# Kernel optimization log

Hardware: AMD Instinct MI355X
Metric: run time of the kernel (lower is better)

Reference implementation:

```python
import jax, jax.numpy as jnp
import numpy as np

L = 2048           # lattice side
R = 2.777          # public-goods multiplier r
GAMMA = 0.8
ETA = 0.8
K_FERMI = 0.5      # fermi temperature used in fermiUpdate


def _plus_sum(x):
    """3x3 plus-kernel conv with circular (wrap) padding == self + 4 rolled neighbors."""
    return (x
            + jnp.roll(x, 1, 0) + jnp.roll(x, -1, 0)
            + jnp.roll(x, 1, 1) + jnp.roll(x, -1, 1))


def setup_inputs() -> dict:
    key = jax.random.key(0)
    k1, k2, k3, k4, k5 = jax.random.split(key, 5)
    return {
        "type_t_minus": jax.random.randint(k1, (L, L), 0, 2, dtype=jnp.int32),
        "type_t": jax.random.randint(k2, (L, L), 0, 2, dtype=jnp.int32),
        "Q_tensor": jax.random.normal(k3, (L * L, 2, 2), dtype=jnp.float32),
        "learning_direction": jax.random.randint(k4, (L, L), 0, 4, dtype=jnp.int32),
        "learning_probabilities": jax.random.uniform(k5, (L, L), dtype=jnp.float32),
    }


def reference(type_t_minus, type_t, Q_tensor, learning_direction, learning_probabilities):
    N = L * L
    # ---- calculation_value: per-cell payoff from the 5 overlapping PGG games ----
    c = (type_t == 1).astype(jnp.float32)   # cooperator mask
    d = (type_t == 0).astype(jnp.float32)   # defector mask
    coop_num = _plus_sum(c)                  # cooperators in own 5-cell group
    base = coop_num * (R / 5.0)
    profit = _plus_sum(base - 1.0) * c + _plus_sum(base) * d   # [L, L]

    # ---- updateQMatrix: Q[C, A, B] <- (1-eta)*Q[C,A,B] + eta*(profit + gamma*max_b Q[C,B,b]) ----
    A = type_t_minus.reshape(-1)             # previous action, [N]
    B = type_t.reshape(-1)                   # current action,  [N]
    Qb = jnp.take_along_axis(Q_tensor, B[:, None, None], axis=1)[:, 0, :]  # Q[C, B, :] -> [N, 2]
    max_values = Qb.max(axis=1)              # [N]
    flatQ = Q_tensor.reshape(N, 4)
    idx = A * 2 + B                          # flattened (A, B) index
    old = jnp.take_along_axis(flatQ, idx[:, None], axis=1)[:, 0]
    upd = (1.0 - ETA) * old + ETA * (profit.reshape(-1) + GAMMA * max_values)
    Q_new = flatQ.at[jnp.arange(N), idx].set(upd).reshape(N, 2, 2)

    # ---- fermiUpdate: gather just-updated Q[C,A,B] (== upd), compare with 4 neighbors ----
    pm = upd.reshape(L, L)                   # fermi profit matrix

    def W(shift, axis):
        return 1.0 / (1.0 + jnp.exp((pm - jnp.roll(pm, shift, axis)) / K_FERMI))

    Ws = jnp.stack([W(1, 1), W(-1, 1), W(1, 0), W(-1, 0)])        # left,right,up,down [4,L,L]
    nb = jnp.stack([jnp.roll(type_t, 1, 1), jnp.roll(type_t, -1, 1),
                    jnp.roll(type_t, 1, 0), jnp.roll(type_t, -1, 0)])
    W_sel = jnp.take_along_axis(Ws, learning_direction[None], axis=0)[0]
    nb_sel = jnp.take_along_axis(nb, learning_direction[None], axis=0)[0]
    type_t1 = jnp.where(learning_probabilities <= W_sel, nb_sel, type_t)  # [L, L] int32

    return (Q_new, type_t1, profit)
```

## Files before the change

kernel.cpp:

```cpp
#include <hip/hip_runtime.h>


#define LSIDE 2048
#define LMASK 2047
#define LSHIFT 11
#define NCELL (LSIDE * LSIDE)

#define TROWS 7
#define TCOLS 264
#define BROWS 5
#define BCOLS 260

__global__ __launch_bounds__(256) void spgg_fused(
    const int* __restrict__ tmin,
    const int* __restrict__ tt,
    const float* __restrict__ Q,
    const int* __restrict__ ldir,
    const float* __restrict__ lp,
    float* __restrict__ Qn,
    float* __restrict__ prof,
    float* __restrict__ t1out)
{
    __shared__ int   tile[TROWS][TCOLS];
    __shared__ float btile[BROWS][BCOLS];

    const int t   = threadIdx.x;
    const int blk = blockIdx.x;
    const int i   = blk >> 3;
    const int j0  = (blk & 7) << 8;
    const int j   = j0 + t;
    const int idx = (i << LSHIFT) + j;

    const int    dir = ldir[idx];
    const float  pv  = lp[idx];
    const float4 qr  = ((const float4*)Q)[idx];
    const int    A   = tmin[idx];

    for (int k = t; k < TROWS * (TCOLS / 4); k += 256) {
        int r = k / (TCOLS / 4);
        int m = k - r * (TCOLS / 4);
        int row_g = (i + r - 3) & LMASK;
        int col_g = (j0 - 4 + (m << 2)) & LMASK;
        int4 v = *(const int4*)&tt[(row_g << LSHIFT) + col_g];
        *(int4*)&tile[r][m << 2] = v;
    }

    const int di = (dir == 3) - (dir == 2);
    const int dj = (dir == 1) - (dir == 0);
    const int ni = (i + di) & LMASK;
    const int nj = (j + dj) & LMASK;
    const int nidx = (ni << LSHIFT) + nj;
    const float4 qn4 = ((const float4*)Q)[nidx];
    const int    An  = tmin[nidx];

    __syncthreads();

    const float KB        = 0.5554f;
    const float ETA       = 0.8f;
    const float ONE_M_ETA = 0.2f;
    const float GAMMA     = 0.8f;

    auto bval = [&](int tr, int tc) -> float {
        int cn = tile[tr][tc] + tile[tr-1][tc] + tile[tr+1][tc]
               + tile[tr][tc-1] + tile[tr][tc+1];
        return __fmul_rn((float)cn, KB);
    };
    #pragma unroll
    for (int r = 0; r < BROWS; ++r)
        btile[r][t] = bval(r + 1, t + 2);
    if (t < BCOLS - 256) {
        #pragma unroll
        for (int r = 0; r < BROWS; ++r)
            btile[r][256 + t] = bval(r + 1, 258 + t);
    }
    __syncthreads();

    auto profit_from_b = [&](int r, int c, int coop) -> float {
        float b_c = btile[r][c];
        float b_u = btile[r-1][c];
        float b_d = btile[r+1][c];
        float b_l = btile[r][c-1];
        float b_r = btile[r][c+1];
        float s0 = __fadd_rn(__fadd_rn(__fadd_rn(__fadd_rn(b_c, b_u), b_d), b_l), b_r);
        float s1 = __fadd_rn(__fadd_rn(__fadd_rn(__fadd_rn(
                       __fsub_rn(b_c, 1.0f), __fsub_rn(b_u, 1.0f)),
                       __fsub_rn(b_d, 1.0f)), __fsub_rn(b_l, 1.0f)),
                       __fsub_rn(b_r, 1.0f));
        return coop ? s1 : s0;
    };

    auto upd_of = [&](float profit, float4 q4, int Ai, int Bi) -> float {
        float q0 = (Bi == 0) ? q4.x : q4.z;
        float q1 = (Bi == 0) ? q4.y : q4.w;
        float mx = fmaxf(q0, q1);
        int k = Ai * 2 + Bi;
        float old = (k == 0) ? q4.x : ((k == 1) ? q4.y : ((k == 2) ? q4.z : q4.w));
        float t0 = __fmul_rn(GAMMA, mx);
        float t1 = __fadd_rn(profit, t0);
        float t2 = __fmul_rn(ETA, t1);
        float t3 = __fmul_rn(ONE_M_ETA, old);
        return __fadd_rn(t3, t2);
    };

    const int B     = tile[3][t + 4];
    float p_own = profit_from_b(2, t + 2, B);
    float upd   = upd_of(p_own, qr, A, B);

    int k = A * 2 + B;
    float4 qo;
    qo.x = (k == 0) ? upd : qr.x;
    qo.y = (k == 1) ? upd : qr.y;
    qo.z = (k == 2) ? upd : qr.z;
    qo.w = (k == 3) ? upd : qr.w;
    ((float4*)Qn)[idx] = qo;
    prof[idx] = p_own;

    const int Bn = tile[3 + di][t + 4 + dj];
    float p_nb   = profit_from_b(2 + di, t + 2 + dj, Bn);
    float upd_nb = upd_of(p_nb, qn4, An, Bn);

    float e1 = __fsub_rn(upd, upd_nb);
    float e2 = __fmul_rn(e1, 2.0f);
    float ex = (float)exp((double)e2);
    float W  = __fdiv_rn(1.0f, __fadd_rn(1.0f, ex));
    int sel = (pv <= W) ? Bn : B;
    t1out[idx] = (float)sel;
}

extern "C" void kernel_launch(void* const* d_in, const int* in_sizes, int n_in,
                              void* d_out, int out_size, void* d_ws, size_t ws_size,
                              hipStream_t stream) {
    const int*   type_t_minus = (const int*)d_in[0];
    const int*   type_t       = (const int*)d_in[1];
    const float* Q_tensor     = (const float*)d_in[2];
    const int*   ldir         = (const int*)d_in[3];
    const float* lprob        = (const float*)d_in[4];

    float* out   = (float*)d_out;
    float* Qn    = out;
    float* t1out = out + (size_t)4 * NCELL;
    float* prof  = out + (size_t)5 * NCELL;

    const int threads = 256;
    const int blocks  = NCELL / threads;
    spgg_fused<<<blocks, threads, 0, stream>>>(type_t_minus, type_t, Q_tensor,
                                               ldir, lprob, Qn, prof, t1out);
}
```

Measured before the change: 220.5 us.

## Process four rows per block and load type tile via direct global-to-LDS

Each block now computes four lattice rows instead of one, sharing a taller halo tile so the redundant halo reads of type_t shrink. The tile is filled with direct global-to-LDS loads, and per-row inputs are batched into registers so more memory requests are in flight. The trade-off is higher register use and lower occupancy. The fill loop also runs past the tile size without a bound check, writing into the btile region before it is computed.

```diff
diff --git a/kernel.cpp b/kernel.cpp
--- a/kernel.cpp
+++ b/kernel.cpp
@@ -6,10 +6,18 @@
 #define LSHIFT 11
 #define NCELL (LSIDE * LSIDE)
 
-#define TROWS 7
+#define CROWS 4
+#define TROWS 10
 #define TCOLS 264
-#define BROWS 5
+#define TI4   66
+#define NI4   (TROWS * TI4)
+#define BROWS 8
 #define BCOLS 260
+#define TILE_INTS (TROWS * TCOLS)
+#define LDS_INTS  (TILE_INTS + BROWS * BCOLS)
+
+typedef __attribute__((address_space(1))) const int gas_int;
+typedef __attribute__((address_space(3))) int las_int;
 
 __global__ __launch_bounds__(256) void spgg_fused(
     const int* __restrict__ tmin,
@@ -21,37 +29,41 @@
     float* __restrict__ prof,
     float* __restrict__ t1out)
 {
-    __shared__ int   tile[TROWS][TCOLS];
-    __shared__ float btile[BROWS][BCOLS];
+    __shared__ __align__(16) int lds_raw[LDS_INTS];
+    int   (*tile)[TCOLS]  = reinterpret_cast<int(*)[TCOLS]>(lds_raw);
+    float (*btile)[BCOLS] = reinterpret_cast<float(*)[BCOLS]>(lds_raw + TILE_INTS);
 
     const int t   = threadIdx.x;
     const int blk = blockIdx.x;
-    const int i   = blk >> 3;
+    const int i0  = (blk >> 3) << 2;
     const int j0  = (blk & 7) << 8;
     const int j   = j0 + t;
-    const int idx = (i << LSHIFT) + j;
+    const int idx0 = (i0 << LSHIFT) + j;
 
-    const int    dir = ldir[idx];
-    const float  pv  = lp[idx];
-    const float4 qr  = ((const float4*)Q)[idx];
-    const int    A   = tmin[idx];
-
-    for (int k = t; k < TROWS * (TCOLS / 4); k += 256) {
-        int r = k / (TCOLS / 4);
-        int m = k - r * (TCOLS / 4);
-        int row_g = (i + r - 3) & LMASK;
-        int col_g = (j0 - 4 + (m << 2)) & LMASK;
-        int4 v = *(const int4*)&tt[(row_g << LSHIFT) + col_g];
-        *(int4*)&tile[r][m << 2] = v;
+    int    dirm[CROWS];
+    float  pvm[CROWS];
+    float4 qrm[CROWS];
+    int    Am[CROWS];
+    #pragma unroll
+    for (int m = 0; m < CROWS; ++m) {
+        int idx = idx0 + (m << LSHIFT);
+        dirm[m] = ldir[idx];
+        pvm[m]  = lp[idx];
+        qrm[m]  = ((const float4*)Q)[idx];
+        Am[m]   = tmin[idx];
     }
 
-    const int di = (dir == 3) - (dir == 2);
-    const int dj = (dir == 1) - (dir == 0);
-    const int ni = (i + di) & LMASK;
-    const int nj = (j + dj) & LMASK;
-    const int nidx = (ni << LSHIFT) + nj;
-    const float4 qn4 = ((const float4*)Q)[nidx];
-    const int    An  = tmin[nidx];
+    #pragma unroll
+    for (int it = 0; it < 3; ++it) {
+        int k = t + (it << 8);
+        int r = k / TI4;
+        int m4 = k - r * TI4;
+        int row_g = (i0 + r - 3) & LMASK;
+        int col_g = (j0 - 4 + (m4 << 2)) & LMASK;
+        __builtin_amdgcn_global_load_lds(
+            (gas_int*)&tt[(row_g << LSHIFT) + col_g],
+            (las_int*)&lds_raw[k << 2], 16, 0, 0);
+    }
 
     __syncthreads();
 
@@ -74,6 +86,18 @@
             btile[r][256 + t] = bval(r + 1, 258 + t);
     }
     __syncthreads();
+
+    int di[CROWS], dj[CROWS];
+    float4 qn4[CROWS];
+    int    An[CROWS];
+    #pragma unroll
+    for (int m = 0; m < CROWS; ++m) {
+        di[m] = (dirm[m] == 3) - (dirm[m] == 2);
+        dj[m] = (dirm[m] == 1) - (dirm[m] == 0);
+        int nidx = ((((i0 + m + di[m]) & LMASK)) << LSHIFT) + ((j + dj[m]) & LMASK);
+        qn4[m] = ((const float4*)Q)[nidx];
+        An[m]  = tmin[nidx];
+    }
 
     auto profit_from_b = [&](int r, int c, int coop) -> float {
         float b_c = btile[r][c];
@@ -102,29 +126,41 @@
         return __fadd_rn(t3, t2);
     };
 
-    const int B     = tile[3][t + 4];
-    float p_own = profit_from_b(2, t + 2, B);
-    float upd   = upd_of(p_own, qr, A, B);
+    int   B[CROWS];
+    float updv[CROWS];
+    #pragma unroll
+    for (int m = 0; m < CROWS; ++m) {
+        B[m] = tile[m + 3][t + 4];
+        float p_own = profit_from_b(m + 2, t + 2, B[m]);
+        updv[m] = upd_of(p_own, qrm[m], Am[m], B[m]);
+        int idx = idx0 + (m << LSHIFT);
+        int k = Am[m] * 2 + B[m];
+        float4 qo;
+        qo.x = (k == 0) ? updv[m] : qrm[m].x;
+        qo.y = (k == 1) ? updv[m] : qrm[m].y;
+        qo.z = (k == 2) ? updv[m] : qrm[m].z;
+        qo.w = (k == 3) ? updv[m] : qrm[m].w;
+        ((float4*)Qn)[idx] = qo;
+        prof[idx] = p_own;
+    }
 
-    int k = A * 2 + B;
-    float4 qo;
-    qo.x = (k == 0) ? upd : qr.x;
-    qo.y = (k == 1) ? upd : qr.y;
-    qo.z = (k == 2) ? upd : qr.z;
-    qo.w = (k == 3) ? upd : qr.w;
-    ((float4*)Qn)[idx] = qo;
-    prof[idx] = p_own;
-
-    const int Bn = tile[3 + di][t + 4 + dj];
-    float p_nb   = profit_from_b(2 + di, t + 2 + dj, Bn);
-    float upd_nb = upd_of(p_nb, qn4, An, Bn);
-
-    float e1 = __fsub_rn(upd, upd_nb);
-    float e2 = __fmul_rn(e1, 2.0f);
-    float ex = (float)exp((double)e2);
-    float W  = __fdiv_rn(1.0f, __fadd_rn(1.0f, ex));
-    int sel = (pv <= W) ? Bn : B;
-    t1out[idx] = (float)sel;
+    float e2[CROWS];
+    int   Bn[CROWS];
+    #pragma unroll
+    for (int m = 0; m < CROWS; ++m) {
+        Bn[m] = tile[m + 3 + di[m]][t + 4 + dj[m]];
+        float p_nb   = profit_from_b(m + 2 + di[m], t + 2 + dj[m], Bn[m]);
+        float upd_nb = upd_of(p_nb, qn4[m], An[m], Bn[m]);
+        float e1 = __fsub_rn(updv[m], upd_nb);
+        e2[m] = __fmul_rn(e1, 2.0f);
+    }
+    #pragma unroll
+    for (int m = 0; m < CROWS; ++m) {
+        float ex = (float)exp((double)e2[m]);
+        float W  = __fdiv_rn(1.0f, __fadd_rn(1.0f, ex));
+        int sel = (pvm[m] <= W) ? Bn[m] : B[m];
+        t1out[idx0 + (m << LSHIFT)] = (float)sel;
+    }
 }
 
 extern "C" void kernel_launch(void* const* d_in, const int* in_sizes, int n_in,
@@ -142,7 +178,7 @@
     float* prof  = out + (size_t)5 * NCELL;
 
     const int threads = 256;
-    const int blocks  = NCELL / threads;
+    const int blocks  = NCELL / (threads * CROWS);
     spgg_fused<<<blocks, threads, 0, stream>>>(type_t_minus, type_t, Q_tensor,
                                                ldir, lprob, Qn, prof, t1out);
 }
```

After: 213.2 us. 3.3% less time.

## Compute four cells per thread from register stencil instead of shared-memory tiles

Applied to the files above, without the earlier changes.

Each thread now handles four consecutive cells. It loads the surrounding type_t stencil straight from global memory into registers, which removes the shared-memory tiles and both block barriers. The thread computes the needed coop-sum and profit values in registers, reuses them to find neighbour profits, and writes outputs with vectorised float4 stores. This trades more redundant global reads per thread and higher register pressure for no LDS traffic, no syncs and wider memory accesses.

```diff
diff --git a/kernel.cpp b/kernel.cpp
--- a/kernel.cpp
+++ b/kernel.cpp
@@ -5,11 +5,6 @@
 #define LMASK 2047
 #define LSHIFT 11
 #define NCELL (LSIDE * LSIDE)
-
-#define TROWS 7
-#define TCOLS 264
-#define BROWS 5
-#define BCOLS 260
 
 __global__ __launch_bounds__(256) void spgg_fused(
     const int* __restrict__ tmin,
@@ -21,66 +16,106 @@
     float* __restrict__ prof,
     float* __restrict__ t1out)
 {
-    __shared__ int   tile[TROWS][TCOLS];
-    __shared__ float btile[BROWS][BCOLS];
-
     const int t   = threadIdx.x;
     const int blk = blockIdx.x;
-    const int i   = blk >> 3;
-    const int j0  = (blk & 7) << 8;
-    const int j   = j0 + t;
-    const int idx = (i << LSHIFT) + j;
-
-    const int    dir = ldir[idx];
-    const float  pv  = lp[idx];
-    const float4 qr  = ((const float4*)Q)[idx];
-    const int    A   = tmin[idx];
-
-    for (int k = t; k < TROWS * (TCOLS / 4); k += 256) {
-        int r = k / (TCOLS / 4);
-        int m = k - r * (TCOLS / 4);
-        int row_g = (i + r - 3) & LMASK;
-        int col_g = (j0 - 4 + (m << 2)) & LMASK;
-        int4 v = *(const int4*)&tt[(row_g << LSHIFT) + col_g];
-        *(int4*)&tile[r][m << 2] = v;
-    }
-
-    const int di = (dir == 3) - (dir == 2);
-    const int dj = (dir == 1) - (dir == 0);
-    const int ni = (i + di) & LMASK;
-    const int nj = (j + dj) & LMASK;
-    const int nidx = (ni << LSHIFT) + nj;
-    const float4 qn4 = ((const float4*)Q)[nidx];
-    const int    An  = tmin[nidx];
-
-    __syncthreads();
+    const int i   = blk >> 1;
+    const int j0  = ((blk & 1) << 10) + (t << 2);
+    const int idx0 = (i << LSHIFT) + j0;
+
+    const int4   dir4 = *(const int4*)&ldir[idx0];
+    const float4 lp4  = *(const float4*)&lp[idx0];
+    const int4   A4   = *(const int4*)&tmin[idx0];
+    float4 qr0 = ((const float4*)Q)[idx0 + 0];
+    float4 qr1 = ((const float4*)Q)[idx0 + 1];
+    float4 qr2 = ((const float4*)Q)[idx0 + 2];
+    float4 qr3 = ((const float4*)Q)[idx0 + 3];
+
+    int rowoff[7];
+    #pragma unroll
+    for (int r = 0; r < 7; ++r) rowoff[r] = ((i + r - 3) & LMASK) << LSHIFT;
+    const int cm4 = (j0 - 4) & LMASK;
+    const int cm2 = (j0 - 2) & LMASK;
+    const int cp4 = (j0 + 4) & LMASK;
+
+    int4 v_m3 = *(const int4*)&tt[rowoff[0] + j0];
+    int2 a_m2 = *(const int2*)&tt[rowoff[1] + cm2];
+    int4 b_m2v= *(const int4*)&tt[rowoff[1] + j0];
+    int  c_m2 =               tt[rowoff[1] + cp4];
+    int2 a_m1 = *(const int2*)&tt[rowoff[2] + cm2];
+    int4 b_m1v= *(const int4*)&tt[rowoff[2] + j0];
+    int2 c_m1 = *(const int2*)&tt[rowoff[2] + cp4];
+    int4 a_0  = *(const int4*)&tt[rowoff[3] + cm4];
+    int4 b_0v = *(const int4*)&tt[rowoff[3] + j0];
+    int4 c_0v = *(const int4*)&tt[rowoff[3] + cp4];
+    int2 a_p1 = *(const int2*)&tt[rowoff[4] + cm2];
+    int4 b_p1v= *(const int4*)&tt[rowoff[4] + j0];
+    int2 c_p1 = *(const int2*)&tt[rowoff[4] + cp4];
+    int2 a_p2 = *(const int2*)&tt[rowoff[5] + cm2];
+    int4 b_p2v= *(const int4*)&tt[rowoff[5] + j0];
+    int  c_p2 =               tt[rowoff[5] + cp4];
+    int4 v_p3 = *(const int4*)&tt[rowoff[6] + j0];
+
+    int di[4], dj[4], An[4];
+    float4 qn4[4];
+    #pragma unroll
+    for (int k = 0; k < 4; ++k) {
+        int dir = (k == 0) ? dir4.x : (k == 1) ? dir4.y : (k == 2) ? dir4.z : dir4.w;
+        di[k] = (dir == 3) - (dir == 2);
+        dj[k] = (dir == 1) - (dir == 0);
+        int nidx = (((i + di[k]) & LMASK) << LSHIFT) + ((j0 + k + dj[k]) & LMASK);
+        qn4[k] = ((const float4*)Q)[nidx];
+        An[k]  = tmin[nidx];
+    }
+
+    int t_m3[4], t_m2[7], t_m1[8], t_0[10], t_p1[8], t_p2[7], t_p3[4];
+    t_m3[0]=v_m3.x; t_m3[1]=v_m3.y; t_m3[2]=v_m3.z; t_m3[3]=v_m3.w;
+    t_m2[0]=a_m2.x; t_m2[1]=a_m2.y; t_m2[2]=b_m2v.x; t_m2[3]=b_m2v.y;
+    t_m2[4]=b_m2v.z; t_m2[5]=b_m2v.w; t_m2[6]=c_m2;
+    t_m1[0]=a_m1.x; t_m1[1]=a_m1.y; t_m1[2]=b_m1v.x; t_m1[3]=b_m1v.y;
+    t_m1[4]=b_m1v.z; t_m1[5]=b_m1v.w; t_m1[6]=c_m1.x; t_m1[7]=c_m1.y;
+    t_0[0]=a_0.y; t_0[1]=a_0.z; t_0[2]=a_0.w;
+    t_0[3]=b_0v.x; t_0[4]=b_0v.y; t_0[5]=b_0v.z; t_0[6]=b_0v.w;
+    t_0[7]=c_0v.x; t_0[8]=c_0v.y; t_0[9]=c_0v.z;
+    t_p1[0]=a_p1.x; t_p1[1]=a_p1.y; t_p1[2]=b_p1v.x; t_p1[3]=b_p1v.y;
+    t_p1[4]=b_p1v.z; t_p1[5]=b_p1v.w; t_p1[6]=c_p1.x; t_p1[7]=c_p1.y;
+    t_p2[0]=a_p2.x; t_p2[1]=a_p2.y; t_p2[2]=b_p2v.x; t_p2[3]=b_p2v.y;
+    t_p2[4]=b_p2v.z; t_p2[5]=b_p2v.w; t_p2[6]=c_p2;
+    t_p3[0]=v_p3.x; t_p3[1]=v_p3.y; t_p3[2]=v_p3.z; t_p3[3]=v_p3.w;
 
     const float KB        = 0.5554f;
     const float ETA       = 0.8f;
     const float ONE_M_ETA = 0.2f;
     const float GAMMA     = 0.8f;
 
-    auto bval = [&](int tr, int tc) -> float {
-        int cn = tile[tr][tc] + tile[tr-1][tc] + tile[tr+1][tc]
-               + tile[tr][tc-1] + tile[tr][tc+1];
-        return __fmul_rn((float)cn, KB);
-    };
-    #pragma unroll
-    for (int r = 0; r < BROWS; ++r)
-        btile[r][t] = bval(r + 1, t + 2);
-    if (t < BCOLS - 256) {
-        #pragma unroll
-        for (int r = 0; r < BROWS; ++r)
-            btile[r][256 + t] = bval(r + 1, 258 + t);
-    }
-    __syncthreads();
-
-    auto profit_from_b = [&](int r, int c, int coop) -> float {
-        float b_c = btile[r][c];
-        float b_u = btile[r-1][c];
-        float b_d = btile[r+1][c];
-        float b_l = btile[r][c-1];
-        float b_r = btile[r][c+1];
+    float b_m2[4], b_m1[6], b_00[8], b_p1[6], b_p2[4];
+    #pragma unroll
+    for (int c = 0; c < 4; ++c) {
+        int cn = t_m2[c+2] + t_m3[c] + t_m1[c+2] + t_m2[c+1] + t_m2[c+3];
+        b_m2[c] = __fmul_rn((float)cn, KB);
+    }
+    #pragma unroll
+    for (int ci = 0; ci < 6; ++ci) {
+        int cn = t_m1[ci+1] + t_m2[ci+1] + t_0[ci+2] + t_m1[ci] + t_m1[ci+2];
+        b_m1[ci] = __fmul_rn((float)cn, KB);
+    }
+    #pragma unroll
+    for (int ci = 0; ci < 8; ++ci) {
+        int cn = t_0[ci+1] + t_m1[ci] + t_p1[ci] + t_0[ci] + t_0[ci+2];
+        b_00[ci] = __fmul_rn((float)cn, KB);
+    }
+    #pragma unroll
+    for (int ci = 0; ci < 6; ++ci) {
+        int cn = t_p1[ci+1] + t_0[ci+2] + t_p2[ci+1] + t_p1[ci] + t_p1[ci+2];
+        b_p1[ci] = __fmul_rn((float)cn, KB);
+    }
+    #pragma unroll
+    for (int c = 0; c < 4; ++c) {
+        int cn = t_p2[c+2] + t_p1[c+2] + t_p3[c] + t_p2[c+1] + t_p2[c+3];
+        b_p2[c] = __fmul_rn((float)cn, KB);
+    }
+
+    auto profit5 = [&](float b_c, float b_u, float b_d, float b_l, float b_r,
+                       int coop) -> float {
         float s0 = __fadd_rn(__fadd_rn(__fadd_rn(__fadd_rn(b_c, b_u), b_d), b_l), b_r);
         float s1 = __fadd_rn(__fadd_rn(__fadd_rn(__fadd_rn(
                        __fsub_rn(b_c, 1.0f), __fsub_rn(b_u, 1.0f)),
@@ -88,6 +123,20 @@
                        __fsub_rn(b_r, 1.0f));
         return coop ? s1 : s0;
     };
+
+    float P0[6], Pm1[4], Pp1[4];
+    #pragma unroll
+    for (int ci = 0; ci < 6; ++ci)
+        P0[ci] = profit5(b_00[ci+1], b_m1[ci], b_p1[ci], b_00[ci], b_00[ci+2],
+                         t_0[ci+2]);
+    #pragma unroll
+    for (int c = 0; c < 4; ++c)
+        Pm1[c] = profit5(b_m1[c+1], b_m2[c], b_00[c+2], b_m1[c], b_m1[c+2],
+                         t_m1[c+2]);
+    #pragma unroll
+    for (int c = 0; c < 4; ++c)
+        Pp1[c] = profit5(b_p1[c+1], b_00[c+2], b_p2[c], b_p1[c], b_p1[c+2],
+                         t_p1[c+2]);
 
     auto upd_of = [&](float profit, float4 q4, int Ai, int Bi) -> float {
         float q0 = (Bi == 0) ? q4.x : q4.z;
@@ -102,29 +151,54 @@
         return __fadd_rn(t3, t2);
     };
 
-    const int B     = tile[3][t + 4];
-    float p_own = profit_from_b(2, t + 2, B);
-    float upd   = upd_of(p_own, qr, A, B);
-
-    int k = A * 2 + B;
-    float4 qo;
-    qo.x = (k == 0) ? upd : qr.x;
-    qo.y = (k == 1) ? upd : qr.y;
-    qo.z = (k == 2) ? upd : qr.z;
-    qo.w = (k == 3) ? upd : qr.w;
-    ((float4*)Qn)[idx] = qo;
-    prof[idx] = p_own;
-
-    const int Bn = tile[3 + di][t + 4 + dj];
-    float p_nb   = profit_from_b(2 + di, t + 2 + dj, Bn);
-    float upd_nb = upd_of(p_nb, qn4, An, Bn);
-
-    float e1 = __fsub_rn(upd, upd_nb);
-    float e2 = __fmul_rn(e1, 2.0f);
-    float ex = (float)exp((double)e2);
-    float W  = __fdiv_rn(1.0f, __fadd_rn(1.0f, ex));
-    int sel = (pv <= W) ? Bn : B;
-    t1out[idx] = (float)sel;
+    int   B[4];
+    float updv[4];
+    #pragma unroll
+    for (int k = 0; k < 4; ++k) {
+        B[k] = t_0[k + 3];
+        int   Ak = (k == 0) ? A4.x : (k == 1) ? A4.y : (k == 2) ? A4.z : A4.w;
+        float4 qk = (k == 0) ? qr0 : (k == 1) ? qr1 : (k == 2) ? qr2 : qr3;
+        updv[k] = upd_of(P0[k + 1], qk, Ak, B[k]);
+        int kk = Ak * 2 + B[k];
+        float4 qo;
+        qo.x = (kk == 0) ? updv[k] : qk.x;
+        qo.y = (kk == 1) ? updv[k] : qk.y;
+        qo.z = (kk == 2) ? updv[k] : qk.z;
+        qo.w = (kk == 3) ? updv[k] : qk.w;
+        ((float4*)Qn)[idx0 + k] = qo;
+    }
+    float4 pr4; pr4.x = P0[1]; pr4.y = P0[2]; pr4.z = P0[3]; pr4.w = P0[4];
+    *(float4*)&prof[idx0] = pr4;
+
+    float e2[4];
+    int   Bn[4];
+    #pragma unroll
+    for (int k = 0; k < 4; ++k) {
+        int dir = (k == 0) ? dir4.x : (k == 1) ? dir4.y : (k == 2) ? dir4.z : dir4.w;
+        float Pn = (dir == 0) ? P0[k]
+                 : (dir == 1) ? P0[k + 2]
+                 : (dir == 2) ? Pm1[k]
+                 :              Pp1[k];
+        Bn[k] = (dir == 0) ? t_0[k + 2]
+              : (dir == 1) ? t_0[k + 4]
+              : (dir == 2) ? t_m1[k + 2]
+              :              t_p1[k + 2];
+        float upd_nb = upd_of(Pn, qn4[k], An[k], Bn[k]);
+        float e1 = __fsub_rn(updv[k], upd_nb);
+        e2[k] = __fmul_rn(e1, 2.0f);
+    }
+    float selv[4];
+    #pragma unroll
+    for (int k = 0; k < 4; ++k) {
+        float ex = (float)exp((double)e2[k]);
+        float W  = __fdiv_rn(1.0f, __fadd_rn(1.0f, ex));
+        float pvk = (k == 0) ? lp4.x : (k == 1) ? lp4.y : (k == 2) ? lp4.z : lp4.w;
+        int sel = (pvk <= W) ? Bn[k] : B[k];
+        selv[k] = (float)sel;
+    }
+    float4 t14;
+    t14.x = selv[0]; t14.y = selv[1]; t14.z = selv[2]; t14.w = selv[3];
+    *(float4*)&t1out[idx0] = t14;
 }
 
 extern "C" void kernel_launch(void* const* d_in, const int* in_sizes, int n_in,
@@ -142,7 +216,7 @@
     float* prof  = out + (size_t)5 * NCELL;
 
     const int threads = 256;
-    const int blocks  = NCELL / threads;
+    const int blocks  = NCELL / (threads * 4);
     spgg_fused<<<blocks, threads, 0, stream>>>(type_t_minus, type_t, Q_tensor,
                                                ldir, lprob, Qn, prof, t1out);
 }
```

Result: slower. 250.0 us (+13.4%).
